# Kernel tuning notes

Measured on AMD Instinct MI355X. Metric: run time of the kernel, lower is better.

## Reference

```python
import jax, jax.numpy as jnp
import numpy as np

D_IN = 1024
D_OUT = 1024
SEQ = 4096


def setup_inputs() -> dict:
    key = jax.random.key(0)
    kx, kq, kk, kv = jax.random.split(key, 4)
    x = jax.random.normal(kx, (SEQ, D_IN), dtype=jnp.float32)
    # torch Linear weights: [d_out, d_in], y = x @ W.T; no bias (qkv_bias=False)
    s = 1.0 / np.sqrt(D_IN)
    Wq = jax.random.uniform(kq, (D_OUT, D_IN), dtype=jnp.float32, minval=-s, maxval=s)
    Wk = jax.random.uniform(kk, (D_OUT, D_IN), dtype=jnp.float32, minval=-s, maxval=s)
    Wv = jax.random.uniform(kv, (D_OUT, D_IN), dtype=jnp.float32, minval=-s, maxval=s)
    return {"x": x, "Wq": Wq, "Wk": Wk, "Wv": Wv}


def reference(x, Wq, Wk, Wv):
    seq = x.shape[0]
    q = x @ Wq.T  # [S, d_out]
    k = x @ Wk.T
    v = x @ Wv.T
    scores = q @ k.T  # [S, S]
    # causal mask: positions j > i masked to -inf (triu, diagonal=1)
    causal = jnp.tril(jnp.ones((seq, seq), dtype=bool))
    scores = jnp.where(causal, scores, -jnp.inf)
    attn = jax.nn.softmax(scores / jnp.sqrt(jnp.float32(q.shape[-1])), axis=-1)
    return attn @ v  # [S, d_out]
```

## Files before the change

### kernel.cpp

```cpp
#include <hip/hip_runtime.h>
#include <hip/hip_bf16.h>
#include <cstdint>
#include <cstddef>


#define SEQQ 4096
#define DDIM 1024

typedef __bf16 bf16x8 __attribute__((ext_vector_type(8)));
typedef float f32x4 __attribute__((ext_vector_type(4)));

__device__ __forceinline__ unsigned short f2bf(float f) {
  unsigned int u = __builtin_bit_cast(unsigned int, f);
  unsigned int r = u + 0x7FFFu + ((u >> 16) & 1u);
  return (unsigned short)(r >> 16);
}

__device__ __forceinline__ void gload_lds16(const void* g, void* lds) {
  __builtin_amdgcn_global_load_lds(
      (__attribute__((address_space(1))) void*)(uintptr_t)g,
      (__attribute__((address_space(3))) void*)(uintptr_t)lds, 16, 0, 0);
}

__global__ __launch_bounds__(256) void cvt_all(const float* __restrict__ x,
                                               const float* __restrict__ Wq,
                                               const float* __restrict__ Wk,
                                               const float* __restrict__ Wv,
                                               unsigned short* __restrict__ xb,
                                               unsigned short* __restrict__ Wcat) {
  int b = blockIdx.x;
  const float* src;
  unsigned short* dst;
  float scale = 1.0f;
  if (b < 4096) {
    src = x; dst = xb;
  } else if (b < 5120) {
    src = Wq; dst = Wcat; scale = 0.03125f; b -= 4096;
  } else if (b < 6144) {
    src = Wk; dst = Wcat + (1u << 20); b -= 5120;
  } else {
    src = Wv; dst = Wcat + (2u << 20); b -= 6144;
  }
  const int i = (b * 256 + threadIdx.x) * 4;
  const float4 v = *reinterpret_cast<const float4*>(src + i);
  ushort4 o;
  o.x = f2bf(v.x * scale);
  o.y = f2bf(v.y * scale);
  o.z = f2bf(v.z * scale);
  o.w = f2bf(v.w * scale);
  *reinterpret_cast<ushort4*>(dst + i) = o;
}

#define GEMM_PRE()                                                          \
  __shared__ unsigned short As[2][32768 / 2] __attribute__((aligned(16)));  \
  __shared__ unsigned short Bs[2][32768 / 2] __attribute__((aligned(16)));  \
  const int tid = threadIdx.x;                                              \
  const int wave = tid >> 6, lane = tid & 63;                               \
  const int wr = (wave >> 2) * 128, wc = (wave & 3) * 64;                   \
  f32x4 acc[8][4] = {};                                                     \
  int offA[8], offB[4];                                                     \
  {                                                                         \
    const int cb = (lane >> 4) * 16;                                        \
    const int rA = wr + (lane & 15);                                        \
    _Pragma("unroll")                                                       \
    for (int m = 0; m < 8; ++m) {                                           \
      int o = (rA + m * 16) * 64 + cb;                                      \
      offA[m] = o ^ (((o >> 9) & 1) << 5);                                  \
    }                                                                       \
    const int rB = wc + (lane & 15);                                        \
    _Pragma("unroll")                                                       \
    for (int n = 0; n < 4; ++n) {                                           \
      int o = (rB + n * 16) * 64 + cb;                                      \
      offB[n] = o ^ (((o >> 9) & 1) << 5);                                  \
    }                                                                       \
  }

#define STAGE(BOFS)                                                         \
  {                                                                         \
    gload_lds16(sA00, ldsA + (BOFS) + dC0);                                 \
    gload_lds16(sA01, ldsA + (BOFS) + dC1);                                 \
    gload_lds16(sA10, ldsA + (BOFS) + 16384 + dC0);                         \
    gload_lds16(sA11, ldsA + (BOFS) + 16384 + dC1);                         \
    gload_lds16(sB00, ldsB + (BOFS) + dC0);                                 \
    gload_lds16(sB01, ldsB + (BOFS) + dC1);                                 \
    gload_lds16(sB10, ldsB + (BOFS) + 16384 + dC0);                         \
    gload_lds16(sB11, ldsB + (BOFS) + 16384 + dC1);                         \
    sA00 += 128; sA01 += 128; sA10 += 128; sA11 += 128;                     \
    sB00 += 128; sB01 += 128; sB10 += 128; sB11 += 128;                     \
  }

#define GEMM_LOOP(ABASE, LDA, BBASE, LDB, S0, S1)                           \
  do {                                                                      \
    const int nt = (S1) - (S0);                                             \
    const size_t lda2 = (size_t)(LDA) * 2, ldb2 = (size_t)(LDB) * 2;        \
    const int r0s = wave * 16 + (lane >> 2);                                \
    const int scb = ((lane & 3) * 16) ^ (((lane >> 5) & 1) << 5);           \
    const char* sA00 = (const char*)(ABASE) + (size_t)r0s * lda2 +          \
                       (size_t)(S0) * 128 + scb;                            \
    const char* sA01 = sA00 + 128 * lda2;                                   \
    const char* sA10 = sA00 + 64;                                           \
    const char* sA11 = sA01 + 64;                                           \
    const char* sB00 = (const char*)(BBASE) + (size_t)r0s * ldb2 +          \
                       (size_t)(S0) * 128 + scb;                            \
    const char* sB01 = sB00 + 128 * ldb2;                                   \
    const char* sB10 = sB00 + 64;                                           \
    const char* sB11 = sB01 + 64;                                           \
    char* ldsA = (char*)&As[0][0];                                          \
    char* ldsB = (char*)&Bs[0][0];                                          \
    const int dC0 = wave * 1024, dC1 = (8 + wave) * 1024;                   \
    STAGE(0);                                                               \
    asm volatile("s_waitcnt vmcnt(0)" ::: "memory");                        \
    asm volatile("s_barrier" ::: "memory");                                 \
    for (int s = 0; s < nt; ++s) {                                          \
      const int bofs = (s & 1) * 32768;                                     \
      bf16x8 a[8], b[4];                                                    \
      _Pragma("unroll")                                                     \
      for (int m = 0; m < 8; ++m)                                           \
        a[m] = *(const bf16x8*)(ldsA + bofs + offA[m]);                     \
      _Pragma("unroll")                                                     \
      for (int n = 0; n < 4; ++n)                                           \
        b[n] = *(const bf16x8*)(ldsB + bofs + offB[n]);                     \
      if (s + 1 < nt) STAGE((~s & 1) * 32768);                              \
      asm volatile("s_waitcnt lgkmcnt(0)" ::: "memory");                    \
      __builtin_amdgcn_sched_barrier(0);                                    \
      __builtin_amdgcn_s_setprio(1);                                        \
      _Pragma("unroll")                                                     \
      for (int m = 0; m < 8; ++m)                                           \
        _Pragma("unroll")                                                   \
        for (int n = 0; n < 4; ++n)                                         \
          acc[m][n] = __builtin_amdgcn_mfma_f32_16x16x32_bf16(              \
              a[m], b[n], acc[m][n], 0, 0, 0);                              \
      __builtin_amdgcn_s_setprio(0);                                        \
      bf16x8 a2[8], b2[4];                                                  \
      _Pragma("unroll")                                                     \
      for (int m = 0; m < 8; ++m)                                           \
        a2[m] = *(const bf16x8*)(ldsA + bofs + 16384 + offA[m]);            \
      _Pragma("unroll")                                                     \
      for (int n = 0; n < 4; ++n)                                           \
        b2[n] = *(const bf16x8*)(ldsB + bofs + 16384 + offB[n]);            \
      asm volatile("s_waitcnt lgkmcnt(0)" ::: "memory");                    \
      __builtin_amdgcn_sched_barrier(0);                                    \
      __builtin_amdgcn_s_setprio(1);                                        \
      _Pragma("unroll")                                                     \
      for (int m = 0; m < 8; ++m)                                           \
        _Pragma("unroll")                                                   \
        for (int n = 0; n < 4; ++n)                                         \
          acc[m][n] = __builtin_amdgcn_mfma_f32_16x16x32_bf16(              \
              a2[m], b2[n], acc[m][n], 0, 0, 0);                            \
      __builtin_amdgcn_s_setprio(0);                                        \
      if (s + 1 < nt) {                                                     \
        asm volatile("s_waitcnt vmcnt(0)" ::: "memory");                    \
        asm volatile("s_barrier" ::: "memory");                             \
      }                                                                     \
    }                                                                       \
  } while (0)

__global__ __launch_bounds__(512, 1) void gemm_qkv(const unsigned short* __restrict__ X,
                                                   const unsigned short* __restrict__ W,
                                                   unsigned short* __restrict__ Qb,
                                                   unsigned short* __restrict__ Kb,
                                                   unsigned short* __restrict__ Vt) {
  GEMM_PRE();
  const int brow = blockIdx.y * 256, bcol = blockIdx.x * 256;
  GEMM_LOOP(X + (size_t)brow * DDIM, DDIM, W + (size_t)bcol * DDIM, DDIM, 0, 16);
  const int region = bcol >> 10;
  const int lcol = bcol & 1023;
  const int c0 = wc + (lane & 15);
  const int r0 = wr + ((lane >> 4) << 2);
  if (region < 2) {
    unsigned short* dst = (region == 0) ? Qb : Kb;
#pragma unroll
    for (int m = 0; m < 8; ++m) {
      const int r = brow + r0 + m * 16;
#pragma unroll
      for (int n = 0; n < 4; ++n) {
        const int c = lcol + c0 + n * 16;
#pragma unroll
        for (int j = 0; j < 4; ++j)
          dst[(size_t)(r + j) * DDIM + c] = f2bf(acc[m][n][j]);
      }
    }
  } else {
#pragma unroll
    for (int m = 0; m < 8; ++m) {
      const int r = brow + r0 + m * 16;
#pragma unroll
      for (int n = 0; n < 4; ++n) {
        const int c = lcol + c0 + n * 16;
        ushort4 pk;
        pk.x = f2bf(acc[m][n][0]);
        pk.y = f2bf(acc[m][n][1]);
        pk.z = f2bf(acc[m][n][2]);
        pk.w = f2bf(acc[m][n][3]);
        *reinterpret_cast<ushort4*>(Vt + (size_t)c * SEQQ + r) = pk;
      }
    }
  }
}

__global__ __launch_bounds__(512, 1) void gemm_qkt(const unsigned short* __restrict__ Qb,
                                                   const unsigned short* __restrict__ Kb,
                                                   unsigned short* __restrict__ S) {
  const int bi = blockIdx.y, bj = blockIdx.x;
  if (bj > bi) return;
  GEMM_PRE();
  const int brow = bi * 256, bcol = bj * 256;
  GEMM_LOOP(Qb + (size_t)brow * DDIM, DDIM, Kb + (size_t)bcol * DDIM, DDIM, 0, 16);
  const int c0 = wc + (lane & 15);
  const int r0 = wr + ((lane >> 4) << 2);
#pragma unroll
  for (int m = 0; m < 8; ++m) {
    const int r = brow + r0 + m * 16;
#pragma unroll
    for (int n = 0; n < 4; ++n) {
      const int c = bcol + c0 + n * 16;
#pragma unroll
      for (int j = 0; j < 4; ++j) {
        unsigned short o = (c > r + j) ? (unsigned short)0xFF80
                                       : f2bf(acc[m][n][j]);
        S[(size_t)(r + j) * SEQQ + c] = o;
      }
    }
  }
}

__global__ __launch_bounds__(256) void softmax_causal(unsigned short* __restrict__ S) {
  const int row = blockIdx.x;
  const int L = ((row >> 8) + 1) << 8;
  unsigned short* Srow = S + (size_t)row * SEQQ;
  __shared__ float red[4];
  const int tid = threadIdx.x;
  const int lane = tid & 63, wave = tid >> 6;

  float x[16];
  bool have[2];
  float m = -3.0e38f;
#pragma unroll
  for (int it = 0; it < 2; ++it) {
    const int j = tid * 8 + it * 2048;
    have[it] = (j < L);
    if (have[it]) {
      const uint4 v = *reinterpret_cast<const uint4*>(Srow + j);
      const unsigned u[4] = {v.x, v.y, v.z, v.w};
#pragma unroll
      for (int q = 0; q < 4; ++q) {
        x[it * 8 + q * 2] = __builtin_bit_cast(float, u[q] << 16);
        x[it * 8 + q * 2 + 1] = __builtin_bit_cast(float, u[q] & 0xFFFF0000u);
      }
#pragma unroll
      for (int q = 0; q < 8; ++q) m = fmaxf(m, x[it * 8 + q]);
    }
  }
#pragma unroll
  for (int o = 32; o; o >>= 1) m = fmaxf(m, __shfl_xor(m, o));
  if (lane == 0) red[wave] = m;
  __syncthreads();
  m = fmaxf(fmaxf(red[0], red[1]), fmaxf(red[2], red[3]));
  __syncthreads();

  float sum = 0.f;
#pragma unroll
  for (int it = 0; it < 2; ++it)
    if (have[it]) {
#pragma unroll
      for (int q = 0; q < 8; ++q) {
        x[it * 8 + q] = __expf(x[it * 8 + q] - m);
        sum += x[it * 8 + q];
      }
    }
#pragma unroll
  for (int o = 32; o; o >>= 1) sum += __shfl_xor(sum, o);
  if (lane == 0) red[wave] = sum;
  __syncthreads();
  sum = red[0] + red[1] + red[2] + red[3];
  const float inv = 1.0f / sum;

#pragma unroll
  for (int it = 0; it < 2; ++it)
    if (have[it]) {
      const int j = tid * 8 + it * 2048;
      unsigned u[4];
#pragma unroll
      for (int q = 0; q < 4; ++q) {
        u[q] = (unsigned)f2bf(x[it * 8 + q * 2] * inv) |
               ((unsigned)f2bf(x[it * 8 + q * 2 + 1] * inv) << 16);
      }
      *reinterpret_cast<uint4*>(Srow + j) = make_uint4(u[0], u[1], u[2], u[3]);
    }
}

__device__ __forceinline__ int pv_nc(int bi) { return (bi >> 2) + 1; }
__device__ __forceinline__ int pv_rcbase(int bi) {
  const int g = bi >> 2, r = bi & 3;
  return 2 * g * (g - 1) + r * g;
}

__global__ __launch_bounds__(512, 1) void gemm_pv_split(const unsigned short* __restrict__ P,
                                                        const unsigned short* __restrict__ Vt,
                                                        float* __restrict__ O,
                                                        float* __restrict__ part) {
  const int bj = blockIdx.x, bi = blockIdx.y, ck = blockIdx.z;
  const int nc = pv_nc(bi);
  if (ck >= nc) return;
  const int kt = (bi + 1) * 4;
  const int W = (kt + nc - 1) / nc;
  const int s0 = ck * W;
  const int s1 = min(s0 + W, kt);
  if (s0 >= s1) return;

  GEMM_PRE();
  const int brow = bi * 256, bcol = bj * 256;
  GEMM_LOOP(P + (size_t)brow * SEQQ, SEQQ, Vt + (size_t)bcol * SEQQ, SEQQ, s0, s1);
  const int c0 = wc + (lane & 15);
  const int r0 = wr + ((lane >> 4) << 2);
  if (ck == 0) {
#pragma unroll
    for (int m = 0; m < 8; ++m) {
      const int r = brow + r0 + m * 16;
#pragma unroll
      for (int n = 0; n < 4; ++n) {
        const int c = bcol + c0 + n * 16;
#pragma unroll
        for (int j = 0; j < 4; ++j)
          O[(size_t)(r + j) * DDIM + c] = acc[m][n][j];
      }
    }
  } else {
    float* tile = part + ((size_t)(pv_rcbase(bi) + (ck - 1)) * 4 + bj) * 65536;
#pragma unroll
    for (int m = 0; m < 8; ++m) {
      const int lr = r0 + m * 16;
#pragma unroll
      for (int n = 0; n < 4; ++n) {
        const int lc = c0 + n * 16;
#pragma unroll
        for (int j = 0; j < 4; ++j)
          tile[(lr + j) * 256 + lc] = acc[m][n][j];
      }
    }
  }
}

__global__ __launch_bounds__(256) void reduce_pv(float* __restrict__ O,
                                                 const float* __restrict__ part) {
  const int idx = blockIdx.x * 256 + threadIdx.x;
  const int r = 1024 + (idx >> 8);
  const int cc = (idx & 255) * 4;
  const int bi = r >> 8;
  const int nparts = bi >> 2;
  const int rcb = pv_rcbase(bi);
  const int bj = cc >> 8;
  const int lr = r & 255, lc = cc & 255;
  float4 acc = *reinterpret_cast<float4*>(O + (size_t)r * DDIM + cc);
  for (int k = 0; k < nparts; ++k) {
    const float4 p = *reinterpret_cast<const float4*>(
        part + ((size_t)(rcb + k) * 4 + bj) * 65536 + lr * 256 + lc);
    acc.x += p.x; acc.y += p.y; acc.z += p.z; acc.w += p.w;
  }
  *reinterpret_cast<float4*>(O + (size_t)r * DDIM + cc) = acc;
}

extern "C" void kernel_launch(void* const* d_in, const int* in_sizes, int n_in,
                              void* d_out, int out_size, void* d_ws, size_t ws_size,
                              hipStream_t stream) {
  (void)in_sizes; (void)n_in; (void)out_size; (void)ws_size;
  const float* x = (const float*)d_in[0];
  const float* Wq = (const float*)d_in[1];
  const float* Wk = (const float*)d_in[2];
  const float* Wv = (const float*)d_in[3];
  float* out = (float*)d_out;

  char* ws = (char*)d_ws;
  unsigned short* xb   = (unsigned short*)(ws);
  unsigned short* Wcat = (unsigned short*)(ws + ((size_t)8 << 20));
  unsigned short* Qb   = (unsigned short*)(ws + ((size_t)14 << 20));
  unsigned short* Kb   = (unsigned short*)(ws + ((size_t)22 << 20));
  unsigned short* Vt   = (unsigned short*)(ws + ((size_t)30 << 20));
  unsigned short* S    = (unsigned short*)(ws + ((size_t)38 << 20));
  float* part = (float*)ws;

  cvt_all<<<7168, 256, 0, stream>>>(x, Wq, Wk, Wv, xb, Wcat);
  gemm_qkv<<<dim3(12, 16), 512, 0, stream>>>(xb, Wcat, Qb, Kb, Vt);
  gemm_qkt<<<dim3(16, 16), 512, 0, stream>>>(Qb, Kb, S);
  softmax_causal<<<SEQQ, 256, 0, stream>>>(S);
  gemm_pv_split<<<dim3(4, 16, 4), 512, 0, stream>>>(S, Vt, out, part);
  reduce_pv<<<3072, 256, 0, stream>>>(out, part);
}
```

Baseline: 130.6 us.

## Restructure GEMM main loop into 8-phase ping-pong schedule with interleaved staging

Replaces the double-buffered GEMM loop, which did two MFMA batches per k-tile and one barrier per tile, with an 8-phase schedule over pairs of k-tiles. Each phase reads a quarter of the fragments, issues a quarter of the next tile's global-to-LDS loads, and runs 16 MFMAs between barriers. Waits are on partial vmcnt counts so memory and compute overlap more finely. The PV split chunk width is rounded to an even number of k-tiles so the loop can step two tiles at a time. This adds many more barriers and needs an even tile count per chunk, which a count such as the qkv GEMM's 16 tiles satisfies.

```diff
diff --git a/kernel.cpp b/kernel.cpp
--- a/kernel.cpp
+++ b/kernel.cpp
@@ -52,8 +52,8 @@
 }
 
 #define GEMM_PRE()                                                          \
-  __shared__ unsigned short As[2][32768 / 2] __attribute__((aligned(16)));  \
-  __shared__ unsigned short Bs[2][32768 / 2] __attribute__((aligned(16)));  \
+  __shared__ unsigned short As[2][16384] __attribute__((aligned(16)));      \
+  __shared__ unsigned short Bs[2][16384] __attribute__((aligned(16)));      \
   const int tid = threadIdx.x;                                              \
   const int wave = tid >> 6, lane = tid & 63;                               \
   const int wr = (wave >> 2) * 128, wc = (wave & 3) * 64;                   \
@@ -75,84 +75,117 @@
     }                                                                       \
   }
 
-#define STAGE(BOFS)                                                         \
-  {                                                                         \
-    gload_lds16(sA00, ldsA + (BOFS) + dC0);                                 \
-    gload_lds16(sA01, ldsA + (BOFS) + dC1);                                 \
-    gload_lds16(sA10, ldsA + (BOFS) + 16384 + dC0);                         \
-    gload_lds16(sA11, ldsA + (BOFS) + 16384 + dC1);                         \
-    gload_lds16(sB00, ldsB + (BOFS) + dC0);                                 \
-    gload_lds16(sB01, ldsB + (BOFS) + dC1);                                 \
-    gload_lds16(sB10, ldsB + (BOFS) + 16384 + dC0);                         \
-    gload_lds16(sB11, ldsB + (BOFS) + 16384 + dC1);                         \
-    sA00 += 128; sA01 += 128; sA10 += 128; sA11 += 128;                     \
-    sB00 += 128; sB01 += 128; sB10 += 128; sB11 += 128;                     \
-  }
-
-#define GEMM_LOOP(ABASE, LDA, BBASE, LDB, S0, S1)                           \
-  do {                                                                      \
-    const int nt = (S1) - (S0);                                             \
-    const size_t lda2 = (size_t)(LDA) * 2, ldb2 = (size_t)(LDB) * 2;        \
-    const int r0s = wave * 16 + (lane >> 2);                                \
-    const int scb = ((lane & 3) * 16) ^ (((lane >> 5) & 1) << 5);           \
-    const char* sA00 = (const char*)(ABASE) + (size_t)r0s * lda2 +          \
-                       (size_t)(S0) * 128 + scb;                            \
-    const char* sA01 = sA00 + 128 * lda2;                                   \
-    const char* sA10 = sA00 + 64;                                           \
-    const char* sA11 = sA01 + 64;                                           \
-    const char* sB00 = (const char*)(BBASE) + (size_t)r0s * ldb2 +          \
-                       (size_t)(S0) * 128 + scb;                            \
-    const char* sB01 = sB00 + 128 * ldb2;                                   \
-    const char* sB10 = sB00 + 64;                                           \
-    const char* sB11 = sB01 + 64;                                           \
-    char* ldsA = (char*)&As[0][0];                                          \
-    char* ldsB = (char*)&Bs[0][0];                                          \
-    const int dC0 = wave * 1024, dC1 = (8 + wave) * 1024;                   \
-    STAGE(0);                                                               \
-    asm volatile("s_waitcnt vmcnt(0)" ::: "memory");                        \
-    asm volatile("s_barrier" ::: "memory");                                 \
-    for (int s = 0; s < nt; ++s) {                                          \
-      const int bofs = (s & 1) * 32768;                                     \
-      bf16x8 a[8], b[4];                                                    \
-      _Pragma("unroll")                                                     \
-      for (int m = 0; m < 8; ++m)                                           \
-        a[m] = *(const bf16x8*)(ldsA + bofs + offA[m]);                     \
-      _Pragma("unroll")                                                     \
-      for (int n = 0; n < 4; ++n)                                           \
-        b[n] = *(const bf16x8*)(ldsB + bofs + offB[n]);                     \
-      if (s + 1 < nt) STAGE((~s & 1) * 32768);                              \
-      asm volatile("s_waitcnt lgkmcnt(0)" ::: "memory");                    \
-      __builtin_amdgcn_sched_barrier(0);                                    \
-      __builtin_amdgcn_s_setprio(1);                                        \
-      _Pragma("unroll")                                                     \
-      for (int m = 0; m < 8; ++m)                                           \
-        _Pragma("unroll")                                                   \
-        for (int n = 0; n < 4; ++n)                                         \
-          acc[m][n] = __builtin_amdgcn_mfma_f32_16x16x32_bf16(              \
-              a[m], b[n], acc[m][n], 0, 0, 0);                              \
-      __builtin_amdgcn_s_setprio(0);                                        \
-      bf16x8 a2[8], b2[4];                                                  \
-      _Pragma("unroll")                                                     \
-      for (int m = 0; m < 8; ++m)                                           \
-        a2[m] = *(const bf16x8*)(ldsA + bofs + 16384 + offA[m]);            \
-      _Pragma("unroll")                                                     \
-      for (int n = 0; n < 4; ++n)                                           \
-        b2[n] = *(const bf16x8*)(ldsB + bofs + 16384 + offB[n]);            \
-      asm volatile("s_waitcnt lgkmcnt(0)" ::: "memory");                    \
-      __builtin_amdgcn_sched_barrier(0);                                    \
-      __builtin_amdgcn_s_setprio(1);                                        \
-      _Pragma("unroll")                                                     \
-      for (int m = 0; m < 8; ++m)                                           \
-        _Pragma("unroll")                                                   \
-        for (int n = 0; n < 4; ++n)                                         \
-          acc[m][n] = __builtin_amdgcn_mfma_f32_16x16x32_bf16(              \
-              a2[m], b2[n], acc[m][n], 0, 0, 0);                            \
-      __builtin_amdgcn_s_setprio(0);                                        \
-      if (s + 1 < nt) {                                                     \
-        asm volatile("s_waitcnt vmcnt(0)" ::: "memory");                    \
-        asm volatile("s_barrier" ::: "memory");                             \
-      }                                                                     \
-    }                                                                       \
+#define BAR asm volatile("s_barrier" ::: "memory")
+
+#define RD_A(SLOT, MH)                                                     \
+  _Pragma("unroll")                                                        \
+  for (int mm = 0; mm < 4; ++mm)                                           \
+    _Pragma("unroll")                                                      \
+    for (int kk = 0; kk < 2; ++kk)                                         \
+      aF[mm][kk] = *(const bf16x8*)(ldsA + (SLOT) * 32768 + kk * 16384 +   \
+                                    offA[(MH) * 4 + mm]);
+
+#define RD_B(SLOT, NP, BS)                                                 \
+  _Pragma("unroll")                                                        \
+  for (int nn = 0; nn < 2; ++nn)                                           \
+    _Pragma("unroll")                                                      \
+    for (int kk = 0; kk < 2; ++kk)                                         \
+      BS[nn][kk] = *(const bf16x8*)(ldsB + (SLOT) * 32768 + kk * 16384 +   \
+                                    offB[(NP) * 2 + nn]);
+
+#define MFMA16(MH, NP, BS)                                                 \
+  __builtin_amdgcn_s_setprio(1);                                           \
+  _Pragma("unroll")                                                        \
+  for (int kk = 0; kk < 2; ++kk)                                           \
+    _Pragma("unroll")                                                      \
+    for (int mm = 0; mm < 4; ++mm)                                         \
+      _Pragma("unroll")                                                    \
+      for (int nn = 0; nn < 2; ++nn)                                       \
+        acc[(MH) * 4 + mm][(NP) * 2 + nn] =                                \
+            __builtin_amdgcn_mfma_f32_16x16x32_bf16(                       \
+                aF[mm][kk], BS[nn][kk],                                    \
+                acc[(MH) * 4 + mm][(NP) * 2 + nn], 0, 0, 0);               \
+  __builtin_amdgcn_s_setprio(0);
+
+#define STGQ(SLOT, KOFS, Q)                                                \
+  {                                                                        \
+    const int lofs = (SLOT) * 32768 + ((Q) & 1) * 16384 + wave * 1024;     \
+    const int sofs = (KOFS) + ((Q) & 1) * 64;                              \
+    if ((Q) < 2) {                                                         \
+      gload_lds16(bA0 + sofs, ldsA + lofs);                                \
+      gload_lds16(bA1 + sofs, ldsA + lofs + 8192);                         \
+    } else {                                                               \
+      gload_lds16(bB0 + sofs, ldsB + lofs);                                \
+      gload_lds16(bB1 + sofs, ldsB + lofs + 8192);                         \
+    }                                                                      \
+  }
+
+#define GEMM_LOOP(ABASE, LDA, BBASE, LDB, S0, S1)                          \
+  do {                                                                     \
+    const int ni = ((S1) - (S0)) >> 1;                                     \
+    const size_t lda2 = (size_t)(LDA) * 2, ldb2 = (size_t)(LDB) * 2;       \
+    const int srow = wave * 16 + (lane >> 2);                              \
+    const int scb = ((lane & 3) * 16) ^ (((lane >> 5) & 1) << 5);          \
+    const char* bA0 = (const char*)(ABASE) + (size_t)srow * lda2 +         \
+                      (size_t)(S0) * 128 + scb;                            \
+    const char* bA1 = bA0 + 128 * lda2;                                    \
+    const char* bB0 = (const char*)(BBASE) + (size_t)srow * ldb2 +         \
+                      (size_t)(S0) * 128 + scb;                            \
+    const char* bB1 = bB0 + 128 * ldb2;                                    \
+    char* ldsA = (char*)&As[0][0];                                         \
+    char* ldsB = (char*)&Bs[0][0];                                         \
+    bf16x8 aF[4][2], b0[2][2], b1[2][2];                                   \
+                                     \
+    STGQ(0, 0, 0); STGQ(0, 0, 1); STGQ(0, 0, 2); STGQ(0, 0, 3);            \
+    STGQ(1, 128, 0);                                                       \
+    asm volatile("s_waitcnt vmcnt(2)" ::: "memory");                       \
+    BAR;                                                                   \
+    for (int i = 0; i < ni; ++i) {                                         \
+      const int k0 = i * 256;                                              \
+      const bool st = (i + 1 < ni);                                        \
+                                                                  \
+      RD_A(0, 0); RD_B(0, 0, b0);                                          \
+      STGQ(1, k0 + 128, 1);                                                \
+      BAR; MFMA16(0, 0, b0); BAR;                                          \
+                                                                  \
+      RD_B(0, 1, b1);                                                      \
+      STGQ(1, k0 + 128, 2);                                                \
+      BAR; MFMA16(0, 1, b1); BAR;                                          \
+                                                                  \
+      RD_A(0, 1);                                                          \
+      STGQ(1, k0 + 128, 3);                                                \
+      BAR; MFMA16(1, 0, b0); BAR;                                          \
+                                                                  \
+      if (st) {                                                            \
+        STGQ(0, k0 + 256, 0);                                              \
+        asm volatile("s_waitcnt vmcnt(2)" ::: "memory");                   \
+      } else {                                                             \
+        asm volatile("s_waitcnt vmcnt(0)" ::: "memory");                   \
+      }                                                                    \
+      BAR; MFMA16(1, 1, b1); BAR;                                          \
+                                                                  \
+      RD_A(1, 0); RD_B(1, 0, b0);                                          \
+      if (st) STGQ(0, k0 + 256, 1);                                        \
+      BAR; MFMA16(0, 0, b0); BAR;                                          \
+                                                                  \
+      RD_B(1, 1, b1);                                                      \
+      if (st) STGQ(0, k0 + 256, 2);                                        \
+      BAR; MFMA16(0, 1, b1); BAR;                                          \
+                                                                  \
+      RD_A(1, 1);                                                          \
+      if (st) STGQ(0, k0 + 256, 3);                                        \
+      BAR; MFMA16(1, 0, b0); BAR;                                          \
+                                                                  \
+      if (st) {                                                            \
+        STGQ(1, k0 + 384, 0);                                              \
+        asm volatile("s_waitcnt vmcnt(2)" ::: "memory");                   \
+        BAR;                                                               \
+        MFMA16(1, 1, b1);                                                  \
+        BAR;                                                               \
+      } else {                                                             \
+        MFMA16(1, 1, b1);                                                  \
+      }                                                                    \
+    }                                                                      \
   } while (0)
 
 __global__ __launch_bounds__(512, 1) void gemm_qkv(const unsigned short* __restrict__ X,
@@ -303,7 +336,7 @@
   const int nc = pv_nc(bi);
   if (ck >= nc) return;
   const int kt = (bi + 1) * 4;
-  const int W = (kt + nc - 1) / nc;
+  const int W = 2 * ((kt + 2 * nc - 1) / (2 * nc));
   const int s0 = ck * W;
   const int s1 = min(s0 + W, kt);
   if (s0 >= s1) return;
```

Result: no change. 128.5 us (-1.6%).
